# Kernel optimization log

Hardware: AMD Instinct MI355X
Metric: run time of the kernel (lower is better)

## Reference

```python
import jax, jax.numpy as jnp
import numpy as np

B, N, D, T = 32, 512, 128, 8
NEG_SLOPE = 0.2
MASK_VAL = -1e10


def _xavier(key, shape, gain=1.0):
    fan_in, fan_out = shape[0], int(np.prod(shape[1:]))
    limit = gain * np.sqrt(6.0 / (fan_in + fan_out))
    return jax.random.uniform(key, shape, jnp.float32, -limit, limit)


def setup_inputs() -> dict:
    key = jax.random.key(0)
    ks = jax.random.split(key, 8)
    atom_embeddings = jax.random.normal(ks[0], (B, N, D), dtype=jnp.float32)
    # bond types in [-1, T-1]; -1 = no bond (masked)
    edges = jax.random.randint(ks[1], (B, N, N), 0, T + 1, dtype=jnp.int64) - 1
    Qw = _xavier(ks[2], (D, D))
    Kw = _xavier(ks[3], (D, D))
    Vw = _xavier(ks[4], (D, D))
    Pw = _xavier(ks[5], (D, D))
    Qb = jnp.zeros((D,), jnp.float32)
    Kb = jnp.zeros((D,), jnp.float32)
    Vb = jnp.zeros((D,), jnp.float32)
    Pb = jnp.zeros((D,), jnp.float32)
    a = _xavier(ks[6], (D, D, T), gain=1.414)
    return {"atom_embeddings": atom_embeddings, "edges": edges,
            "Qw": Qw, "Qb": Qb, "Kw": Kw, "Kb": Kb, "Vw": Vw, "Vb": Vb,
            "a": a, "Pw": Pw, "Pb": Pb}


def reference(atom_embeddings, edges, Qw, Qb, Kw, Kb, Vw, Vb, a, Pw, Pb):
    # torch Linear: x @ W.T + b
    src = atom_embeddings @ Qw.T + Qb            # (B,N,D)
    dst = atom_embeddings @ Kw.T + Kb            # (B,N,D)
    val = atom_embeddings @ Vw.T + Vb            # (B,N,D)

    # bilinear edge-type scores: s[b,n,m,t] = src[b,n,:] @ a[:,:,t] @ dst[b,m,:]
    ts = jnp.einsum('bnd,det->bnet', src, a)     # (B,N,D,T)
    scores = jnp.einsum('bnet,bme->bnmt', ts, dst)  # (B,N,N,T)

    # gather the slice for each edge's bond type (clamp -1 -> 0 like torch)
    idx = jnp.clip(edges, 0, None)[..., None]    # (B,N,N,1)
    att = jnp.take_along_axis(scores, idx, axis=-1)[..., 0]  # (B,N,N)
    att = jnp.where(edges == -1, MASK_VAL, att)
    att = jnp.where(att >= 0, att, NEG_SLOPE * att)  # leaky_relu
    att = jax.nn.softmax(att, axis=-1)           # (B,N,N)

    out = att @ val                              # (B,N,D)
    return out @ Pw.T + Pb
```

## Files before the change

kernel.cpp:

```cpp
#include <hip/hip_runtime.h>
#include <stdint.h>


typedef short bf16x8 __attribute__((ext_vector_type(8)));
typedef float f32x4 __attribute__((ext_vector_type(4)));
typedef unsigned short u16;
typedef unsigned int u32;
typedef unsigned long long u64;

__device__ __forceinline__ u16 f2bf(float x) {
    union { float f; u32 u; } v; v.f = x;
    u32 r = v.u + 0x7FFFu + ((v.u >> 16) & 1u);
    return (u16)(r >> 16);
}
__device__ __forceinline__ float bf2f(u16 h) {
    union { u32 u; float f; } v; v.u = ((u32)h) << 16; return v.f;
}
__device__ __forceinline__ void split_hl(float x, u16& h, u16& l) {
    h = f2bf(x);
    l = f2bf(x - bf2f(h));
}
__device__ __forceinline__ void split4(float4 x, u64& hq, u64& lq) {
    u16 h0, l0, h1, l1, h2, l2, h3, l3;
    split_hl(x.x, h0, l0); split_hl(x.y, h1, l1);
    split_hl(x.z, h2, l2); split_hl(x.w, h3, l3);
    hq = (u64)h0 | ((u64)h1 << 16) | ((u64)h2 << 32) | ((u64)h3 << 48);
    lq = (u64)l0 | ((u64)l1 << 16) | ((u64)l2 << 32) | ((u64)l3 << 48);
}
__device__ __forceinline__ void split8(float4 a, float4 b, bf16x8& h8, bf16x8& l8) {
    u16 hh[8], ll[8];
    split_hl(a.x, hh[0], ll[0]); split_hl(a.y, hh[1], ll[1]);
    split_hl(a.z, hh[2], ll[2]); split_hl(a.w, hh[3], ll[3]);
    split_hl(b.x, hh[4], ll[4]); split_hl(b.y, hh[5], ll[5]);
    split_hl(b.z, hh[6], ll[6]); split_hl(b.w, hh[7], ll[7]);
    #pragma unroll
    for (int i = 0; i < 8; i++) { h8[i] = (short)hh[i]; l8[i] = (short)ll[i]; }
}
__device__ __forceinline__ f32x4 mfma16(bf16x8 a, bf16x8 b, f32x4 c) {
    return __builtin_amdgcn_mfma_f32_16x16x32_bf16(a, b, c, 0, 0, 0);
}

__global__ void prep_kernel(const float* __restrict__ Qw, const float* __restrict__ Qb,
                            const float* __restrict__ Kw, const float* __restrict__ Kb,
                            const float* __restrict__ Vw, const float* __restrict__ Vb,
                            const float* __restrict__ Aa, const float* __restrict__ Pw,
                            u16* __restrict__ WFH, u16* __restrict__ WFL,
                            float* __restrict__ bcat) {
    int gid = blockIdx.x * 256 + threadIdx.x;
    if (gid >= 1280 * 128) return;
    int j = gid >> 7, d = gid & 127;
    float v, bias = 0.f;
    if (j < 128) { v = Kw[j * 128 + d]; bias = Kb[j]; }
    else if (j < 256) {
        int jj = j - 128;
        float s = 0.f, bs = 0.f;
        for (int k = 0; k < 128; k++) {
            float p = Pw[jj * 128 + k];
            s += p * Vw[k * 128 + d];
            bs += p * Vb[k];
        }
        v = s; bias = bs;
    } else {
        int r = j - 256, t = r >> 7, jj = r & 127;
        float s = 0.f, bs = 0.f;
        for (int e = 0; e < 128; e++) {
            float av = Aa[(e * 128 + jj) * 8 + t];
            s += Qw[e * 128 + d] * av;
            bs += Qb[e] * av;
        }
        v = s; bias = bs;
    }
    u16 h, l; split_hl(v, h, l);
    size_t idx = ((size_t)((j >> 4) * 16 + (d >> 3)) * 16 + (j & 15)) * 8 + (d & 7);
    WFH[idx] = h; WFL[idx] = l;
    if (d == 0) bcat[j] = bias;
}

__global__ void detect_kernel(const int* __restrict__ E, int* __restrict__ flag) {
    __shared__ int bad;
    if (threadIdx.x == 0) bad = 0;
    __syncthreads();
    int w0 = E[2 * threadIdx.x + 1];
    int w1 = E[2 * (threadIdx.x + 256) + 1];
    if (!(w0 == 0 || w0 == -1) || !(w1 == 0 || w1 == -1)) atomicOr(&bad, 1);
    __syncthreads();
    if (threadIdx.x == 0) *flag = (bad ? 0 : 1);
}

__launch_bounds__(256, 3)
__global__ void gemm1_kernel(const float* __restrict__ X,
                             const u16* __restrict__ WFH, const u16* __restrict__ WFL,
                             const float* __restrict__ bcat,
                             float* __restrict__ C,
                             u16* __restrict__ VTH, u16* __restrict__ VTL) {
    const int id = blockIdx.x;
    const int xcd = id & 7, q = id >> 3;
    const int g0 = (xcd * 32 + (q >> 2)) * 64;
    const int jsplit = q & 3;
    const int tid = threadIdx.x;
    const int wid = tid >> 6, lane = tid & 63;
    const int gblk = (wid >> 1) * 32, jblk = (wid & 1) * 32;
    const int lr = lane & 15, lg = lane >> 4;

    bf16x8 afh[4][2], afl[4][2];
    #pragma unroll
    for (int ks = 0; ks < 4; ks++)
    #pragma unroll
    for (int r = 0; r < 2; r++) {
        const float* p = X + (size_t)(g0 + gblk + r * 16 + lr) * 128 + ks * 32 + lg * 8;
        float4 a = *(const float4*)p;
        float4 b = *(const float4*)(p + 4);
        split8(a, b, afh[ks][r], afl[ks][r]);
    }

    #pragma unroll
    for (int jt5 = 0; jt5 < 5; jt5++) {
        const int jt = jsplit * 5 + jt5;
        const int j0 = jt * 64;
        const bool valTile = (jt == 2 || jt == 3);
        const int jgbase = (j0 + jblk) >> 4;
        f32x4 acc[2][2] = {};
        if (valTile) {
            #pragma unroll
            for (int ks = 0; ks < 4; ks++) {
                bf16x8 bfh[2], bfl[2];
                #pragma unroll
                for (int c = 0; c < 2; c++) {
                    size_t eo = ((size_t)((jgbase + c) * 16 + ks * 4 + lg) * 16 + lr) * 8;
                    bfh[c] = *(const bf16x8*)(WFH + eo);
                    bfl[c] = *(const bf16x8*)(WFL + eo);
                }
                #pragma unroll
                for (int r = 0; r < 2; r++)
                #pragma unroll
                for (int c = 0; c < 2; c++) {
                    acc[r][c] = mfma16(afh[ks][r], bfh[c], acc[r][c]);
                    acc[r][c] = mfma16(afh[ks][r], bfl[c], acc[r][c]);
                    acc[r][c] = mfma16(afl[ks][r], bfh[c], acc[r][c]);
                }
            }
            const int b = g0 >> 9;
            #pragma unroll
            for (int r = 0; r < 2; r++)
            #pragma unroll
            for (int c = 0; c < 2; c++) {
                int j = j0 + jblk + c * 16 + lr;
                float bias = bcat[j];
                int d = j - 128;
                int n = (g0 & 511) + gblk + r * 16 + 4 * lg;
                float4 v = {acc[r][c][0] + bias, acc[r][c][1] + bias,
                            acc[r][c][2] + bias, acc[r][c][3] + bias};
                u64 hq, lq; split4(v, hq, lq);
                size_t off = ((size_t)(b * 128 + d)) * 512 + n;
                *(u64*)(VTH + off) = hq;
                *(u64*)(VTL + off) = lq;
            }
        } else {
            #pragma unroll
            for (int ks = 0; ks < 4; ks++) {
                bf16x8 bfh[2], bfl[2];
                #pragma unroll
                for (int c = 0; c < 2; c++) {
                    size_t eo = ((size_t)((jgbase + c) * 16 + ks * 4 + lg) * 16 + lr) * 8;
                    bfh[c] = *(const bf16x8*)(WFH + eo);
                    bfl[c] = *(const bf16x8*)(WFL + eo);
                }
                #pragma unroll
                for (int c = 0; c < 2; c++)
                #pragma unroll
                for (int r = 0; r < 2; r++) {
                    acc[c][r] = mfma16(bfh[c], afh[ks][r], acc[c][r]);
                    acc[c][r] = mfma16(bfh[c], afl[ks][r], acc[c][r]);
                    acc[c][r] = mfma16(bfl[c], afh[ks][r], acc[c][r]);
                }
            }
            #pragma unroll
            for (int c = 0; c < 2; c++)
            #pragma unroll
            for (int r = 0; r < 2; r++) {
                int j = j0 + jblk + c * 16 + 4 * lg;
                int g = g0 + gblk + r * 16 + lr;
                float4 bias4 = *(const float4*)(bcat + j);
                float4 v = {acc[c][r][0] + bias4.x, acc[c][r][1] + bias4.y,
                            acc[c][r][2] + bias4.z, acc[c][r][3] + bias4.w};
                *(float4*)(C + (size_t)g * 1280 + j) = v;
            }
        }
    }
}

__launch_bounds__(512, 2)
__global__ void scores_kernel(const float* __restrict__ C,
                              const void* __restrict__ Eptr, const int* __restrict__ flag,
                              float* __restrict__ att) {
    const int id = blockIdx.x;
    const int xcd = id & 7, j = id >> 3;
    const int m0 = (j & 3) * 128;
    const int pair = xcd * 32 + (j >> 2);
    const int n0 = (pair & 7) * 64, b = pair >> 3;
    __shared__ u16 BH[128 * 128], BL[128 * 128];
    __shared__ u16 AH[2][64 * 128], AL[2][64 * 128];
    const int tid = threadIdx.x;
    const int wid = tid >> 6, lane = tid & 63;
    const int wr = (wid >> 2) * 32, wc = (wid & 3) * 32;
    const int lr = lane & 15, lg = lane >> 4;
    const bool e64 = (*flag != 0);

    #pragma unroll
    for (int i = 0; i < 8; i++) {
        int idx = tid + i * 512;
        int row = idx >> 5, c4 = idx & 31;
        float4 x = *(const float4*)(C + (size_t)(b * 512 + m0 + row) * 1280 + c4 * 4);
        u64 hq, lq; split4(x, hq, lq);
        int boff = (row * 256 + c4 * 8) ^ ((row & 7) << 4);
        *(u64*)((char*)BH + boff) = hq;
        *(u64*)((char*)BL + boff) = lq;
    }
    int ed[2][2][4];
    #pragma unroll
    for (int r = 0; r < 2; r++)
    #pragma unroll
    for (int c = 0; c < 2; c++)
    #pragma unroll
    for (int q = 0; q < 4; q++) {
        size_t n = n0 + wr + r * 16 + 4 * lg + q;
        size_t m = m0 + wc + c * 16 + lr;
        size_t idx = ((size_t)b * 512 + n) * 512 + m;
        ed[r][c][q] = e64 ? (int)((const long long*)Eptr)[idx] : ((const int*)Eptr)[idx];
    }
    {
        #pragma unroll
        for (int i = 0; i < 4; i++) {
            int idx = tid + i * 512;
            int row = idx >> 5, c4 = idx & 31;
            float4 x = *(const float4*)(C + (size_t)(b * 512 + n0 + row) * 1280 + 256 + c4 * 4);
            u64 hq, lq; split4(x, hq, lq);
            int boff = (row * 256 + c4 * 8) ^ ((row & 7) << 4);
            *(u64*)((char*)AH[0] + boff) = hq;
            *(u64*)((char*)AL[0] + boff) = lq;
        }
    }
    __syncthreads();
    bf16x8 bfh[4][2], bfl[4][2];
    #pragma unroll
    for (int ks = 0; ks < 4; ks++) {
        const int kb2 = (ks * 32 + lg * 8) * 2;
        #pragma unroll
        for (int c = 0; c < 2; c++) {
            int row = wc + c * 16 + lr;
            int boff = (row * 256 + kb2) ^ ((row & 7) << 4);
            bfh[ks][c] = *(const bf16x8*)((const char*)BH + boff);
            bfl[ks][c] = *(const bf16x8*)((const char*)BL + boff);
        }
    }
    float sel[2][2][4];
    #pragma unroll
    for (int r = 0; r < 2; r++)
    #pragma unroll
    for (int c = 0; c < 2; c++)
    #pragma unroll
    for (int q = 0; q < 4; q++) sel[r][c][q] = 0.f;

    for (int t = 0; t < 8; t++) {
        const int cur = t & 1;
        float4 nx[4];
        if (t < 7) {
            #pragma unroll
            for (int i = 0; i < 4; i++) {
                int idx = tid + i * 512;
                int row = idx >> 5, c4 = idx & 31;
                nx[i] = *(const float4*)(C + (size_t)(b * 512 + n0 + row) * 1280
                                           + 256 + (t + 1) * 128 + c4 * 4);
            }
        }
        f32x4 acc[2][2] = {};
        __builtin_amdgcn_s_setprio(1);
        #pragma unroll
        for (int ks = 0; ks < 4; ks++) {
            const int kb2 = (ks * 32 + lg * 8) * 2;
            bf16x8 afh[2], afl[2];
            #pragma unroll
            for (int r = 0; r < 2; r++) {
                int row = wr + r * 16 + lr;
                int boff = (row * 256 + kb2) ^ ((row & 7) << 4);
                afh[r] = *(const bf16x8*)((const char*)AH[cur] + boff);
                afl[r] = *(const bf16x8*)((const char*)AL[cur] + boff);
            }
            #pragma unroll
            for (int r = 0; r < 2; r++)
            #pragma unroll
            for (int c = 0; c < 2; c++) {
                acc[r][c] = mfma16(afh[r], bfh[ks][c], acc[r][c]);
                acc[r][c] = mfma16(afh[r], bfl[ks][c], acc[r][c]);
                acc[r][c] = mfma16(afl[r], bfh[ks][c], acc[r][c]);
            }
        }
        __builtin_amdgcn_s_setprio(0);
        #pragma unroll
        for (int r = 0; r < 2; r++)
        #pragma unroll
        for (int c = 0; c < 2; c++)
        #pragma unroll
        for (int q = 0; q < 4; q++) {
            int ec = ed[r][c][q] < 0 ? 0 : ed[r][c][q];
            sel[r][c][q] = (ec == t) ? acc[r][c][q] : sel[r][c][q];
        }
        if (t < 7) {
            #pragma unroll
            for (int i = 0; i < 4; i++) {
                int idx = tid + i * 512;
                int row = idx >> 5, c4 = idx & 31;
                u64 hq, lq; split4(nx[i], hq, lq);
                int boff = (row * 256 + c4 * 8) ^ ((row & 7) << 4);
                *(u64*)((char*)AH[cur ^ 1] + boff) = hq;
                *(u64*)((char*)AL[cur ^ 1] + boff) = lq;
            }
        }
        __syncthreads();
    }
    #pragma unroll
    for (int r = 0; r < 2; r++)
    #pragma unroll
    for (int c = 0; c < 2; c++)
    #pragma unroll
    for (int q = 0; q < 4; q++) {
        float v = (ed[r][c][q] == -1) ? -1e10f : sel[r][c][q];
        v = (v >= 0.f) ? v : 0.2f * v;
        size_t n = n0 + wr + r * 16 + 4 * lg + q;
        size_t m = m0 + wc + c * 16 + lr;
        att[((size_t)b * 512 + n) * 512 + m] = v;
    }
}

__launch_bounds__(256, 2)
__global__ void out_kernel(const float* __restrict__ att,
                           const u16* __restrict__ VTH, const u16* __restrict__ VTL,
                           const float* __restrict__ Pb, float* __restrict__ out) {
    const int id = blockIdx.x;
    const int xcd = id & 7, j = id >> 3;
    const int b = xcd * 4 + (j >> 4);
    const int n0 = (j & 15) * 32;
    __shared__ u16 PH[32 * 64], PL[32 * 64];
    __shared__ u16 VH[128 * 64], VL[128 * 64];
    const int tid = threadIdx.x;
    const int row = tid >> 3, c8 = tid & 7;
    float4 av0[8], av1[8];
    const float4* rp = (const float4*)(att + ((size_t)b * 512 + n0 + row) * 512);
    #pragma unroll
    for (int mc = 0; mc < 8; mc++) {
        av0[mc] = rp[mc * 16 + c8 * 2];
        av1[mc] = rp[mc * 16 + c8 * 2 + 1];
    }
    float mx = -1e30f;
    #pragma unroll
    for (int mc = 0; mc < 8; mc++) {
        mx = fmaxf(mx, fmaxf(fmaxf(fmaxf(av0[mc].x, av0[mc].y), fmaxf(av0[mc].z, av0[mc].w)),
                             fmaxf(fmaxf(av1[mc].x, av1[mc].y), fmaxf(av1[mc].z, av1[mc].w))));
    }
    #pragma unroll
    for (int o = 1; o < 8; o <<= 1) mx = fmaxf(mx, __shfl_xor(mx, o, 64));
    float s = 0.f;
    #pragma unroll
    for (int mc = 0; mc < 8; mc++) {
        av0[mc].x = expf(av0[mc].x - mx); av0[mc].y = expf(av0[mc].y - mx);
        av0[mc].z = expf(av0[mc].z - mx); av0[mc].w = expf(av0[mc].w - mx);
        av1[mc].x = expf(av1[mc].x - mx); av1[mc].y = expf(av1[mc].y - mx);
        av1[mc].z = expf(av1[mc].z - mx); av1[mc].w = expf(av1[mc].w - mx);
        s += av0[mc].x + av0[mc].y + av0[mc].z + av0[mc].w
           + av1[mc].x + av1[mc].y + av1[mc].z + av1[mc].w;
    }
    #pragma unroll
    for (int o = 1; o < 8; o <<= 1) s += __shfl_xor(s, o, 64);
    const float inv = 1.0f / s;
    const int wid = tid >> 6, lane = tid & 63;
    const int lr = lane & 15, lg = lane >> 4;
    const int wc = wid * 32;
    f32x4 acc[2][2] = {};
    for (int mc = 0; mc < 8; mc++) {
        {
            float4 p0 = {av0[mc].x * inv, av0[mc].y * inv, av0[mc].z * inv, av0[mc].w * inv};
            float4 p1 = {av1[mc].x * inv, av1[mc].y * inv, av1[mc].z * inv, av1[mc].w * inv};
            u64 h0, l0, h1, l1;
            split4(p0, h0, l0); split4(p1, h1, l1);
            int boff = (row * 128 + c8 * 16) ^ ((row & 7) << 4);
            *(u64*)((char*)PH + boff) = h0;
            *(u64*)((char*)PH + boff + 8) = h1;
            *(u64*)((char*)PL + boff) = l0;
            *(u64*)((char*)PL + boff + 8) = l1;
        }
        #pragma unroll
        for (int i = 0; i < 4; i++) {
            int idx = tid + i * 256;
            int vrow = idx >> 3, ch = idx & 7;
            size_t src = ((size_t)(b * 128 + vrow)) * 512 + mc * 64;
            int boff = (vrow * 128 + ch * 16) ^ ((vrow & 7) << 4);
            *(uint4*)((char*)VH + boff) = ((const uint4*)(VTH + src))[ch];
            *(uint4*)((char*)VL + boff) = ((const uint4*)(VTL + src))[ch];
        }
        __syncthreads();
        #pragma unroll
        for (int ks = 0; ks < 2; ks++) {
            const int kb2 = (ks * 32 + lg * 8) * 2;
            bf16x8 ah[2], al[2];
            #pragma unroll
            for (int r = 0; r < 2; r++) {
                int prow = r * 16 + lr;
                int boff = (prow * 128 + kb2) ^ ((prow & 7) << 4);
                ah[r] = *(const bf16x8*)((const char*)PH + boff);
                al[r] = *(const bf16x8*)((const char*)PL + boff);
            }
            #pragma unroll
            for (int c = 0; c < 2; c++) {
                int vrow = wc + c * 16 + lr;
                int boff = (vrow * 128 + kb2) ^ ((vrow & 7) << 4);
                bf16x8 bh = *(const bf16x8*)((const char*)VH + boff);
                bf16x8 bl = *(const bf16x8*)((const char*)VL + boff);
                #pragma unroll
                for (int r = 0; r < 2; r++) {
                    acc[r][c] = mfma16(ah[r], bh, acc[r][c]);
                    acc[r][c] = mfma16(ah[r], bl, acc[r][c]);
                    acc[r][c] = mfma16(al[r], bh, acc[r][c]);
                }
            }
        }
        __syncthreads();
    }
    #pragma unroll
    for (int r = 0; r < 2; r++)
    #pragma unroll
    for (int c = 0; c < 2; c++)
    #pragma unroll
    for (int q = 0; q < 4; q++) {
        int n = n0 + r * 16 + 4 * lg + q;
        int d = wc + c * 16 + lr;
        out[((size_t)b * 512 + n) * 128 + d] = acc[r][c][q] + Pb[d];
    }
}

extern "C" void kernel_launch(void* const* d_in, const int* in_sizes, int n_in,
                              void* d_out, int out_size, void* d_ws, size_t ws_size,
                              hipStream_t stream) {
    (void)in_sizes; (void)n_in; (void)out_size; (void)ws_size;
    const float* X  = (const float*)d_in[0];
    const void*  E  = d_in[1];
    const float* Qw = (const float*)d_in[2];
    const float* Qb = (const float*)d_in[3];
    const float* Kw = (const float*)d_in[4];
    const float* Kb = (const float*)d_in[5];
    const float* Vw = (const float*)d_in[6];
    const float* Vb = (const float*)d_in[7];
    const float* Aa = (const float*)d_in[8];
    const float* Pw = (const float*)d_in[9];
    const float* Pb = (const float*)d_in[10];
    float* out = (float*)d_out;

    char* ws = (char*)d_ws;
    size_t cur = 0;
    auto alloc = [&](size_t bytes) -> char* {
        char* p = ws + cur;
        cur += (bytes + 255) & ~(size_t)255;
        return p;
    };
    int*   flag = (int*)  alloc(4);
    u16*   WFH  = (u16*)  alloc((size_t)1280 * 128 * 2);
    u16*   WFL  = (u16*)  alloc((size_t)1280 * 128 * 2);
    float* bcat = (float*)alloc(1280 * 4);
    float* C    = (float*)alloc((size_t)16384 * 1280 * 4);
    u16*   VTH  = (u16*)  alloc((size_t)32 * 128 * 512 * 2);
    u16*   VTL  = (u16*)  alloc((size_t)32 * 128 * 512 * 2);
    float* att  = (float*)alloc((size_t)32 * 512 * 512 * 4);

    prep_kernel<<<640, 256, 0, stream>>>(Qw, Qb, Kw, Kb, Vw, Vb, Aa, Pw, WFH, WFL, bcat);
    detect_kernel<<<1, 256, 0, stream>>>((const int*)E, flag);
    gemm1_kernel<<<1024, 256, 0, stream>>>(X, WFH, WFL, bcat, C, VTH, VTL);
    scores_kernel<<<1024, 512, 0, stream>>>(C, E, flag, att);
    out_kernel<<<512, 256, 0, stream>>>(att, VTH, VTL, Pb, out);
}
```

Measured before the change: 221.3 us.

## Emit pre-split bf16 fragment layouts from gemm1 and drop LDS staging in scores

gemm1 now converts its fp32 results to hi/lo bf16 pairs and writes them in an MFMA-fragment-ordered layout, replacing the fp32 C matrix. scores_kernel then loads its operands straight from global memory in fragment order, with no shared-memory staging, no repeated splitting and no barriers. It also moves to 64x64 tiles with 256 threads and twice as many blocks. This cuts intermediate bytes and conversion work, but operand reuse now depends on L2/L1 rather than LDS, and the t-loop is no longer software-pipelined.

```diff
diff --git a/kernel.cpp b/kernel.cpp
--- a/kernel.cpp
+++ b/kernel.cpp
@@ -91,7 +91,8 @@
 __global__ void gemm1_kernel(const float* __restrict__ X,
                              const u16* __restrict__ WFH, const u16* __restrict__ WFL,
                              const float* __restrict__ bcat,
-                             float* __restrict__ C,
+                             u16* __restrict__ FSH, u16* __restrict__ FSL,
+                             u16* __restrict__ FBH, u16* __restrict__ FBL,
                              u16* __restrict__ VTH, u16* __restrict__ VTL) {
     const int id = blockIdx.x;
     const int xcd = id & 7, q = id >> 3;
@@ -112,6 +113,7 @@
         float4 b = *(const float4*)(p + 4);
         split8(a, b, afh[ks][r], afl[ks][r]);
     }
+    const int b = g0 >> 9;
 
     #pragma unroll
     for (int jt5 = 0; jt5 < 5; jt5++) {
@@ -139,7 +141,6 @@
                     acc[r][c] = mfma16(afl[ks][r], bfh[c], acc[r][c]);
                 }
             }
-            const int b = g0 >> 9;
             #pragma unroll
             for (int r = 0; r < 2; r++)
             #pragma unroll
@@ -174,48 +175,68 @@
                     acc[c][r] = mfma16(bfl[c], afh[ks][r], acc[c][r]);
                 }
             }
-            #pragma unroll
-            for (int c = 0; c < 2; c++)
-            #pragma unroll
-            for (int r = 0; r < 2; r++) {
-                int j = j0 + jblk + c * 16 + 4 * lg;
-                int g = g0 + gblk + r * 16 + lr;
-                float4 bias4 = *(const float4*)(bcat + j);
-                float4 v = {acc[c][r][0] + bias4.x, acc[c][r][1] + bias4.y,
-                            acc[c][r][2] + bias4.z, acc[c][r][3] + bias4.w};
-                *(float4*)(C + (size_t)g * 1280 + j) = v;
-            }
-        }
-    }
-}
-
-__launch_bounds__(512, 2)
-__global__ void scores_kernel(const float* __restrict__ C,
+            if (jt < 2) {
+                const int mt = (g0 & 511) >> 7;
+                const int mbase = g0 & 127;
+                size_t fb = (size_t)(b * 4 + mt) * 16384;
+                #pragma unroll
+                for (int c = 0; c < 2; c++)
+                #pragma unroll
+                for (int r = 0; r < 2; r++) {
+                    int d0 = j0 + jblk + c * 16 + 4 * lg;
+                    float4 bias4 = *(const float4*)(bcat + d0);
+                    float4 v = {acc[c][r][0] + bias4.x, acc[c][r][1] + bias4.y,
+                                acc[c][r][2] + bias4.z, acc[c][r][3] + bias4.w};
+                    u64 hq, lq; split4(v, hq, lq);
+                    int kc = (d0 >> 5) * 4 + ((d0 >> 3) & 3);
+                    int mrow = mbase + gblk + r * 16 + lr;
+                    size_t off = fb + ((size_t)kc * 128 + mrow) * 8 + (d0 & 7);
+                    *(u64*)(FBH + off) = hq;
+                    *(u64*)(FBL + off) = lq;
+                }
+            } else {
+                const int nt = (g0 & 511) >> 6;
+                const int tt = (jt - 4) >> 1;
+                size_t fs = ((size_t)(b * 8 + nt) * 8 + tt) * 8192;
+                #pragma unroll
+                for (int c = 0; c < 2; c++)
+                #pragma unroll
+                for (int r = 0; r < 2; r++) {
+                    int j = j0 + jblk + c * 16 + 4 * lg;
+                    float4 bias4 = *(const float4*)(bcat + j);
+                    float4 v = {acc[c][r][0] + bias4.x, acc[c][r][1] + bias4.y,
+                                acc[c][r][2] + bias4.z, acc[c][r][3] + bias4.w};
+                    u64 hq, lq; split4(v, hq, lq);
+                    int d0 = ((jt - 4) & 1) * 64 + jblk + c * 16 + 4 * lg;
+                    int kc = (d0 >> 5) * 4 + ((d0 >> 3) & 3);
+                    int nrow = gblk + r * 16 + lr;
+                    size_t off = fs + ((size_t)kc * 64 + nrow) * 8 + (d0 & 7);
+                    *(u64*)(FSH + off) = hq;
+                    *(u64*)(FSL + off) = lq;
+                }
+            }
+        }
+    }
+}
+
+__launch_bounds__(256, 3)
+__global__ void scores_kernel(const u16* __restrict__ FSH, const u16* __restrict__ FSL,
+                              const u16* __restrict__ FBH, const u16* __restrict__ FBL,
                               const void* __restrict__ Eptr, const int* __restrict__ flag,
                               float* __restrict__ att) {
     const int id = blockIdx.x;
-    const int xcd = id & 7, j = id >> 3;
-    const int m0 = (j & 3) * 128;
-    const int pair = xcd * 32 + (j >> 2);
-    const int n0 = (pair & 7) * 64, b = pair >> 3;
-    __shared__ u16 BH[128 * 128], BL[128 * 128];
-    __shared__ u16 AH[2][64 * 128], AL[2][64 * 128];
+    const int xcd = id & 7, s = id >> 3;
+    const int b = xcd * 4 + (s >> 6);
+    const int tile = s & 63;
+    const int n0 = (tile >> 3) * 64, m0 = (tile & 7) * 64;
+    const int nt = n0 >> 6;
+    const int mt = m0 >> 7, mb = m0 & 127;
     const int tid = threadIdx.x;
     const int wid = tid >> 6, lane = tid & 63;
-    const int wr = (wid >> 2) * 32, wc = (wid & 3) * 32;
+    const int wr = (wid >> 1) * 32, wc = (wid & 1) * 32;
     const int lr = lane & 15, lg = lane >> 4;
     const bool e64 = (*flag != 0);
 
-    #pragma unroll
-    for (int i = 0; i < 8; i++) {
-        int idx = tid + i * 512;
-        int row = idx >> 5, c4 = idx & 31;
-        float4 x = *(const float4*)(C + (size_t)(b * 512 + m0 + row) * 1280 + c4 * 4);
-        u64 hq, lq; split4(x, hq, lq);
-        int boff = (row * 256 + c4 * 8) ^ ((row & 7) << 4);
-        *(u64*)((char*)BH + boff) = hq;
-        *(u64*)((char*)BL + boff) = lq;
-    }
     int ed[2][2][4];
     #pragma unroll
     for (int r = 0; r < 2; r++)
@@ -228,30 +249,15 @@
         size_t idx = ((size_t)b * 512 + n) * 512 + m;
         ed[r][c][q] = e64 ? (int)((const long long*)Eptr)[idx] : ((const int*)Eptr)[idx];
     }
-    {
-        #pragma unroll
-        for (int i = 0; i < 4; i++) {
-            int idx = tid + i * 512;
-            int row = idx >> 5, c4 = idx & 31;
-            float4 x = *(const float4*)(C + (size_t)(b * 512 + n0 + row) * 1280 + 256 + c4 * 4);
-            u64 hq, lq; split4(x, hq, lq);
-            int boff = (row * 256 + c4 * 8) ^ ((row & 7) << 4);
-            *(u64*)((char*)AH[0] + boff) = hq;
-            *(u64*)((char*)AL[0] + boff) = lq;
-        }
-    }
-    __syncthreads();
     bf16x8 bfh[4][2], bfl[4][2];
     #pragma unroll
-    for (int ks = 0; ks < 4; ks++) {
-        const int kb2 = (ks * 32 + lg * 8) * 2;
-        #pragma unroll
-        for (int c = 0; c < 2; c++) {
-            int row = wc + c * 16 + lr;
-            int boff = (row * 256 + kb2) ^ ((row & 7) << 4);
-            bfh[ks][c] = *(const bf16x8*)((const char*)BH + boff);
-            bfl[ks][c] = *(const bf16x8*)((const char*)BL + boff);
-        }
+    for (int ks = 0; ks < 4; ks++)
+    #pragma unroll
+    for (int c = 0; c < 2; c++) {
+        size_t eo = (size_t)(b * 4 + mt) * 16384
+                  + ((size_t)((ks * 4 + lg) * 128 + mb + wc + c * 16 + lr)) * 8;
+        bfh[ks][c] = *(const bf16x8*)(FBH + eo);
+        bfl[ks][c] = *(const bf16x8*)(FBL + eo);
     }
     float sel[2][2][4];
     #pragma unroll
@@ -261,30 +267,19 @@
     #pragma unroll
     for (int q = 0; q < 4; q++) sel[r][c][q] = 0.f;
 
+    const size_t abase0 = (size_t)(b * 8 + nt) * 8 * 8192;
+    #pragma unroll 1
     for (int t = 0; t < 8; t++) {
-        const int cur = t & 1;
-        float4 nx[4];
-        if (t < 7) {
-            #pragma unroll
-            for (int i = 0; i < 4; i++) {
-                int idx = tid + i * 512;
-                int row = idx >> 5, c4 = idx & 31;
-                nx[i] = *(const float4*)(C + (size_t)(b * 512 + n0 + row) * 1280
-                                           + 256 + (t + 1) * 128 + c4 * 4);
-            }
-        }
+        const size_t abase = abase0 + (size_t)t * 8192;
         f32x4 acc[2][2] = {};
-        __builtin_amdgcn_s_setprio(1);
         #pragma unroll
         for (int ks = 0; ks < 4; ks++) {
-            const int kb2 = (ks * 32 + lg * 8) * 2;
             bf16x8 afh[2], afl[2];
             #pragma unroll
             for (int r = 0; r < 2; r++) {
-                int row = wr + r * 16 + lr;
-                int boff = (row * 256 + kb2) ^ ((row & 7) << 4);
-                afh[r] = *(const bf16x8*)((const char*)AH[cur] + boff);
-                afl[r] = *(const bf16x8*)((const char*)AL[cur] + boff);
+                size_t eo = abase + ((size_t)((ks * 4 + lg) * 64 + wr + r * 16 + lr)) * 8;
+                afh[r] = *(const bf16x8*)(FSH + eo);
+                afl[r] = *(const bf16x8*)(FSL + eo);
             }
             #pragma unroll
             for (int r = 0; r < 2; r++)
@@ -295,7 +290,6 @@
                 acc[r][c] = mfma16(afl[r], bfh[ks][c], acc[r][c]);
             }
         }
-        __builtin_amdgcn_s_setprio(0);
         #pragma unroll
         for (int r = 0; r < 2; r++)
         #pragma unroll
@@ -305,18 +299,6 @@
             int ec = ed[r][c][q] < 0 ? 0 : ed[r][c][q];
             sel[r][c][q] = (ec == t) ? acc[r][c][q] : sel[r][c][q];
         }
-        if (t < 7) {
-            #pragma unroll
-            for (int i = 0; i < 4; i++) {
-                int idx = tid + i * 512;
-                int row = idx >> 5, c4 = idx & 31;
-                u64 hq, lq; split4(nx[i], hq, lq);
-                int boff = (row * 256 + c4 * 8) ^ ((row & 7) << 4);
-                *(u64*)((char*)AH[cur ^ 1] + boff) = hq;
-                *(u64*)((char*)AL[cur ^ 1] + boff) = lq;
-            }
-        }
-        __syncthreads();
     }
     #pragma unroll
     for (int r = 0; r < 2; r++)
@@ -465,14 +447,17 @@
     u16*   WFH  = (u16*)  alloc((size_t)1280 * 128 * 2);
     u16*   WFL  = (u16*)  alloc((size_t)1280 * 128 * 2);
     float* bcat = (float*)alloc(1280 * 4);
-    float* C    = (float*)alloc((size_t)16384 * 1280 * 4);
+    u16*   FSH  = (u16*)  alloc((size_t)32 * 8 * 8 * 8192 * 2);
+    u16*   FSL  = (u16*)  alloc((size_t)32 * 8 * 8 * 8192 * 2);
+    u16*   FBH  = (u16*)  alloc((size_t)32 * 4 * 16384 * 2);
+    u16*   FBL  = (u16*)  alloc((size_t)32 * 4 * 16384 * 2);
     u16*   VTH  = (u16*)  alloc((size_t)32 * 128 * 512 * 2);
     u16*   VTL  = (u16*)  alloc((size_t)32 * 128 * 512 * 2);
     float* att  = (float*)alloc((size_t)32 * 512 * 512 * 4);
 
     prep_kernel<<<640, 256, 0, stream>>>(Qw, Qb, Kw, Kb, Vw, Vb, Aa, Pw, WFH, WFL, bcat);
     detect_kernel<<<1, 256, 0, stream>>>((const int*)E, flag);
-    gemm1_kernel<<<1024, 256, 0, stream>>>(X, WFH, WFL, bcat, C, VTH, VTL);
-    scores_kernel<<<1024, 512, 0, stream>>>(C, E, flag, att);
+    gemm1_kernel<<<1024, 256, 0, stream>>>(X, WFH, WFL, bcat, FSH, FSL, FBH, FBL, VTH, VTL);
+    scores_kernel<<<2048, 256, 0, stream>>>(FSH, FSL, FBH, FBL, E, flag, att);
     out_kernel<<<512, 256, 0, stream>>>(att, VTH, VTL, Pb, out);
 }
```

After: 242.7 us. +9.7%, slower.
